# Performance work log

Measured on AMD Instinct MI355X. Metric: run time of the kernel, lower is better.

Reference implementation:

```python
import jax, jax.numpy as jnp
import numpy as np

IN_C, HID, OUT_C, N = 128, 128, 1, 8192


def setup_inputs() -> dict:
    key = jax.random.key(0)
    ks = jax.random.split(key, 16)
    s_in = 1.0 / np.sqrt(IN_C)
    s_h = 1.0 / np.sqrt(HID)
    inp = {
        "x": jax.random.normal(ks[0], (N, IN_C), dtype=jnp.float32),
        "Wq": jax.random.uniform(ks[1], (IN_C, HID), minval=-s_in, maxval=s_in),
        "bq": jnp.zeros((HID,), jnp.float32),
        "Wk": jax.random.uniform(ks[2], (IN_C, HID), minval=-s_in, maxval=s_in),
        "bk": jnp.zeros((HID,), jnp.float32),
        "Wv": jax.random.uniform(ks[3], (IN_C, HID), minval=-s_in, maxval=s_in),
        "bv": jnp.zeros((HID,), jnp.float32),
        "Wskip": jax.random.uniform(ks[4], (IN_C, HID), minval=-s_in, maxval=s_in),
        "bskip": jnp.zeros((HID,), jnp.float32),
        "W1": jax.random.uniform(ks[5], (HID, HID), minval=-s_h, maxval=s_h),
        "b1": jnp.zeros((HID,), jnp.float32),
        "W2": jax.random.uniform(ks[6], (HID, OUT_C), minval=-s_h, maxval=s_h),
        "b2": jnp.zeros((OUT_C,), jnp.float32),
        "k": 7,
    }
    return inp


def _transformer_conv(x, Wq, bq, Wk, bk, Wv, bv, Wskip, bskip):
    # PyG TransformerConv, heads=1, concat=False, root_weight=True, over a
    # complete graph (no self-loops) -> dense attention with masked diagonal.
    q = x @ Wq + bq  # [N, H]
    kk = x @ Wk + bk
    v = x @ Wv + bv
    d = q.shape[-1]
    scores = (q @ kk.T) / jnp.sqrt(jnp.asarray(d, q.dtype))  # [N, N]
    n = x.shape[0]
    eye = jnp.eye(n, dtype=bool)
    scores = jnp.where(eye, -jnp.inf, scores)
    attn = jax.nn.softmax(scores, axis=-1)
    out = attn @ v
    return out + x @ Wskip + bskip


def _knn_indices(h, k):
    # k nearest neighbors (excluding self) in squared-euclidean distance.
    sq = jnp.sum(h * h, axis=1)
    d2 = sq[:, None] + sq[None, :] - 2.0 * (h @ h.T)  # [N, N]
    n = h.shape[0]
    d2 = jnp.where(jnp.eye(n, dtype=bool), jnp.inf, d2)
    _, idx = jax.lax.top_k(-d2, k)  # [N, k] neighbor (source) indices
    return idx


def _gcn_conv(h, idx, W, b, k):
    # Each node has exactly k incoming edges + self-loop => gcn_norm weight
    # is uniformly 1/(k+1) on every edge.
    m = h @ W  # [N, d]
    agg = (m[idx].sum(axis=1) + m) / jnp.asarray(k + 1, h.dtype)
    return agg + b


def reference(x, Wq, bq, Wk, bk, Wv, bv, Wskip, bskip, W1, b1, W2, b2, k):
    h = _transformer_conv(x, Wq, bq, Wk, bk, Wv, bv, Wskip, bskip)  # [N, HID]
    idx = _knn_indices(h, k)  # KNNGraph(k) on embeddings
    h1 = jax.nn.relu(_gcn_conv(h, idx, W1, b1, k))
    out = _gcn_conv(h1, idx, W2, b2, k)  # [N, OUT_C]
    return out
```

## Files before the change

kernel.cpp:

```cpp
#include <hip/hip_runtime.h>
#include <cmath>


typedef unsigned short ushort_t;

constexpr int   NN    = 8192;
constexpr int   DD    = 128;
constexpr int   KNB   = 7;
constexpr int   NL    = 10;
constexpr int   NCAND = 12;
constexpr float SCALE = 0.088388347648318447f;

using bf16x8 = __attribute__((ext_vector_type(8))) short;
using f32x4  = __attribute__((ext_vector_type(4))) float;

#define MFMA16(a, b, c) __builtin_amdgcn_mfma_f32_16x16x32_bf16((a), (b), (c), 0, 0, 0)

__device__ __forceinline__ ushort_t f2b(float f) {
    union { float f; unsigned int u; } v; v.f = f;
    return (ushort_t)((v.u + 0x8000u) >> 16);
}
__device__ __forceinline__ float b2f(ushort_t h) {
    union { unsigned int u; float f; } v; v.u = ((unsigned int)h) << 16;
    return v.f;
}

__device__ __forceinline__ void gload16(const void* g, void* l) {
    __builtin_amdgcn_global_load_lds(
        (const __attribute__((address_space(1))) unsigned int*)g,
        (__attribute__((address_space(3))) unsigned int*)l, 16, 0, 0);
}

__device__ __forceinline__ unsigned umin_(unsigned a, unsigned b) { return a < b ? a : b; }
__device__ __forceinline__ unsigned umax_(unsigned a, unsigned b) { return a > b ? a : b; }

template<int K>
__device__ __forceinline__ void ins_asc(unsigned* a, unsigned x)
{
    #pragma unroll
    for (int p = K - 1; p >= 1; --p)
        a[p] = umin_(umax_(x, a[p - 1]), a[p]);
    a[0] = umin_(a[0], x);
}

__global__ __launch_bounds__(128)
void proj_kernel(const float* __restrict__ x,
                 const float* __restrict__ Wq, const float* __restrict__ bq,
                 const float* __restrict__ Wk, const float* __restrict__ bk,
                 const float* __restrict__ Wv, const float* __restrict__ bv,
                 const float* __restrict__ Ws, const float* __restrict__ bs,
                 ushort_t* __restrict__ Qhi, ushort_t* __restrict__ Qlo,
                 ushort_t* __restrict__ Khi, ushort_t* __restrict__ Klo,
                 float* __restrict__ Vf, float* __restrict__ HS)
{
    __shared__ float xs[4][DD];
    const int i0 = blockIdx.x * 4, t = threadIdx.x;
    #pragma unroll
    for (int r = 0; r < 4; ++r) xs[r][t] = x[(i0 + r) * DD + t];
    __syncthreads();
    float aq[4] = {0,0,0,0}, ak[4] = {0,0,0,0}, av[4] = {0,0,0,0}, ah[4] = {0,0,0,0};
    #pragma unroll 4
    for (int c = 0; c < DD; ++c) {
        const float wq = Wq[c * DD + t], wk = Wk[c * DD + t];
        const float wv = Wv[c * DD + t], ws = Ws[c * DD + t];
        #pragma unroll
        for (int r = 0; r < 4; ++r) {
            const float xv = xs[r][c];
            aq[r] = fmaf(xv, wq, aq[r]); ak[r] = fmaf(xv, wk, ak[r]);
            av[r] = fmaf(xv, wv, av[r]); ah[r] = fmaf(xv, ws, ah[r]);
        }
    }
    #pragma unroll
    for (int r = 0; r < 4; ++r) {
        const int o = (i0 + r) * DD + t;
        const float q = aq[r] + bq[t];
        const float k = ak[r] + bk[t];
        const ushort_t qh = f2b(q); Qhi[o] = qh; Qlo[o] = f2b(q - b2f(qh));
        const ushort_t kh = f2b(k); Khi[o] = kh; Klo[o] = f2b(k - b2f(kh));
        Vf[o] = av[r] + bv[t];
        HS[o] = ah[r] + bs[t];
    }
}

__global__ __launch_bounds__(256)
void vt_kernel(const float* __restrict__ Vf,
               ushort_t* __restrict__ VThi, ushort_t* __restrict__ VTlo)
{
    __shared__ float tile[64 * 132];
    const int k0 = blockIdx.x * 64, t = threadIdx.x;
    #pragma unroll
    for (int p = 0; p < 8; ++p) {
        const int slot = t + p * 256;
        const int r = slot >> 5, c4 = slot & 31;
        *reinterpret_cast<float4*>(&tile[r * 132 + c4 * 4]) =
            *reinterpret_cast<const float4*>(Vf + (k0 + r) * DD + c4 * 4);
    }
    __syncthreads();
    #pragma unroll
    for (int p = 0; p < 4; ++p) {
        const int slot = t + p * 256;
        const int f = slot >> 3, kc = slot & 7;
        ushort_t hh[8], ll[8];
        #pragma unroll
        for (int i = 0; i < 8; ++i) {
            const float v = tile[(kc * 8 + i) * 132 + f];
            hh[i] = f2b(v); ll[i] = f2b(v - b2f(hh[i]));
        }
        *reinterpret_cast<uint4*>(VThi + f * NN + k0 + kc * 8) =
            *reinterpret_cast<const uint4*>(hh);
        *reinterpret_cast<uint4*>(VTlo + f * NN + k0 + kc * 8) =
            *reinterpret_cast<const uint4*>(ll);
    }
}

constexpr int ANS  = 8;
constexpr int AKS  = NN / ANS;
constexpr int BK   = 32;
constexpr int PSTR = 40;
constexpr int KSTR = 136;

__global__ __launch_bounds__(256, 2)
void attn_kernel(const ushort_t* __restrict__ Qhi, const ushort_t* __restrict__ Qlo,
                 const ushort_t* __restrict__ Khg, const ushort_t* __restrict__ Klg,
                 const ushort_t* __restrict__ Vhg, const ushort_t* __restrict__ Vlg,
                 float* __restrict__ Opart, float* __restrict__ lpart)
{
    __shared__ __align__(16) ushort_t Khs[2][BK * DD];
    __shared__ __align__(16) ushort_t Kls[2][BK * DD];
    __shared__ __align__(16) ushort_t Vhs[2][DD * BK];
    __shared__ __align__(16) ushort_t Vls[2][DD * BK];
    __shared__ __align__(16) ushort_t Phs[4][16 * PSTR];
    __shared__ __align__(16) ushort_t Pls[4][16 * PSTR];

    const int t  = threadIdx.x;
    const int w  = t >> 6, l = t & 63;
    const int lc = l & 15, lq = l >> 4;
    const int b  = blockIdx.x;
    const int s  = b >> 6;
    const int qb = b & 63;
    const int i0 = qb * 128;
    const int k0 = s * AKS;
    ushort_t* Pwh = Phs[w];
    ushort_t* Pwl = Pls[w];

    const int lrK = w * 4 + (l >> 4);
    const int kchunk = ((l & 15) ^ (lrK & 7)) * 8;
    const ushort_t* gKh = Khg + (size_t)(k0 + lrK) * DD + kchunk;
    const ushort_t* gKl = Klg + (size_t)(k0 + lrK) * DD + kchunk;
    const int lrV = w * 16 + (l >> 2);
    const int vchunk = ((l & 3) ^ ((l >> 3) & 3)) * 8;
    const ushort_t* gVh = Vhg + (size_t)lrV * NN + k0 + vchunk;
    const ushort_t* gVl = Vlg + (size_t)lrV * NN + k0 + vchunk;

#define STAGE_K(buf, koff) do {                                              \
    gload16(gKh + (size_t)(koff) * DD,        &Khs[buf][(w * 4) * DD]);      \
    gload16(gKh + (size_t)((koff) + 16) * DD, &Khs[buf][(16 + w * 4) * DD]); \
    gload16(gKl + (size_t)(koff) * DD,        &Kls[buf][(w * 4) * DD]);      \
    gload16(gKl + (size_t)((koff) + 16) * DD, &Kls[buf][(16 + w * 4) * DD]); \
  } while (0)
#define STAGE_V(buf, koff) do {                                              \
    gload16(gVh + (koff),                     &Vhs[buf][(w * 16) * BK]);     \
    gload16(gVh + (size_t)64 * NN + (koff),   &Vhs[buf][(64 + w * 16) * BK]);\
    gload16(gVl + (koff),                     &Vls[buf][(w * 16) * BK]);     \
    gload16(gVl + (size_t)64 * NN + (koff),   &Vls[buf][(64 + w * 16) * BK]);\
  } while (0)

    bf16x8 qh[2][4], ql[2][4];
    #pragma unroll
    for (int sub = 0; sub < 2; ++sub) {
        const int row = i0 + w * 32 + sub * 16 + lc;
        #pragma unroll
        for (int kb = 0; kb < 4; ++kb) {
            qh[sub][kb] = *reinterpret_cast<const bf16x8*>(Qhi + row * DD + kb * 32 + lq * 8);
            ql[sub][kb] = *reinterpret_cast<const bf16x8*>(Qlo + row * DD + kb * 32 + lq * 8);
        }
    }

    const f32x4 zz = {0.f, 0.f, 0.f, 0.f};
    f32x4 oacc[2][8];
    #pragma unroll
    for (int sub = 0; sub < 2; ++sub)
        #pragma unroll
        for (int ft = 0; ft < 8; ++ft) oacc[sub][ft] = zz;
    float lrow[2] = {0.f, 0.f};

    bf16x8 pah[2] = {}, pal[2] = {};
    const int vc = (lq ^ ((lc >> 1) & 3)) * 8;

    STAGE_K(0, 0);
    __syncthreads();

    constexpr int NT = AKS / BK;
    for (int it = 0; it < NT; ++it) {
        const int cur = it & 1;
        const int jt  = k0 + it * BK;

        if (it + 1 < NT) STAGE_K(cur ^ 1, (it + 1) * BK);
        STAGE_V(cur, it * BK);

        const ushort_t* Kh = Khs[cur];
        const ushort_t* Kl = Kls[cur];

        f32x4 sacc[2][2];
        #pragma unroll
        for (int sub = 0; sub < 2; ++sub)
            #pragma unroll
            for (int kt = 0; kt < 2; ++kt) sacc[sub][kt] = zz;
        __builtin_amdgcn_s_setprio(1);
        #pragma unroll
        for (int kt = 0; kt < 2; ++kt) {
            const int kro = (kt * 16 + lc) * DD;
            #pragma unroll
            for (int kb = 0; kb < 4; ++kb) {
                const int cp = ((kb * 4 + lq) ^ (lc & 7)) * 8;
                const bf16x8 kh = *reinterpret_cast<const bf16x8*>(&Kh[kro + cp]);
                const bf16x8 kl = *reinterpret_cast<const bf16x8*>(&Kl[kro + cp]);
                #pragma unroll
                for (int sub = 0; sub < 2; ++sub) {
                    sacc[sub][kt] = MFMA16(kh, qh[sub][kb], sacc[sub][kt]);
                    sacc[sub][kt] = MFMA16(kh, ql[sub][kb], sacc[sub][kt]);
                    sacc[sub][kt] = MFMA16(kl, qh[sub][kb], sacc[sub][kt]);
                }
            }
        }
        __builtin_amdgcn_s_setprio(0);

        if (it > 0) {
            const ushort_t* Vh = Vhs[cur ^ 1];
            const ushort_t* Vl = Vls[cur ^ 1];
            __builtin_amdgcn_s_setprio(1);
            #pragma unroll
            for (int ft = 0; ft < 8; ++ft) {
                const bf16x8 vh = *reinterpret_cast<const bf16x8*>(
                    &Vh[(ft * 16 + lc) * BK + vc]);
                const bf16x8 vl = *reinterpret_cast<const bf16x8*>(
                    &Vl[(ft * 16 + lc) * BK + vc]);
                #pragma unroll
                for (int sub = 0; sub < 2; ++sub) {
                    oacc[sub][ft] = MFMA16(pah[sub], vh, oacc[sub][ft]);
                    oacc[sub][ft] = MFMA16(pal[sub], vh, oacc[sub][ft]);
                    oacc[sub][ft] = MFMA16(pah[sub], vl, oacc[sub][ft]);
                }
            }
            __builtin_amdgcn_s_setprio(0);
        }

        if ((jt & ~127) == i0) {
            #pragma unroll
            for (int sub = 0; sub < 2; ++sub) {
                const int gq = i0 + w * 32 + sub * 16 + lc;
                #pragma unroll
                for (int kt = 0; kt < 2; ++kt)
                    #pragma unroll
                    for (int r = 0; r < 4; ++r) {
                        const int gk = jt + kt * 16 + lq * 4 + r;
                        if (gk == gq) sacc[sub][kt][r] = -INFINITY;
                    }
            }
        }
        #pragma unroll
        for (int sub = 0; sub < 2; ++sub) {
            #pragma unroll
            for (int kt = 0; kt < 2; ++kt) {
                unsigned wh[2], wl[2];
                #pragma unroll
                for (int rr = 0; rr < 2; ++rr) {
                    const float p0 = __expf(sacc[sub][kt][rr * 2 + 0] * SCALE);
                    const float p1 = __expf(sacc[sub][kt][rr * 2 + 1] * SCALE);
                    lrow[sub] += p0;
                    lrow[sub] += p1;
                    const ushort_t ph0 = f2b(p0), ph1 = f2b(p1);
                    wh[rr] = (unsigned)ph0 | ((unsigned)ph1 << 16);
                    wl[rr] = (unsigned)f2b(p0 - b2f(ph0)) |
                             ((unsigned)f2b(p1 - b2f(ph1)) << 16);
                }
                const int eo = lc * PSTR + kt * 16 + lq * 4;
                *reinterpret_cast<uint2*>(&Pwh[eo]) = make_uint2(wh[0], wh[1]);
                *reinterpret_cast<uint2*>(&Pwl[eo]) = make_uint2(wl[0], wl[1]);
            }
            pah[sub] = *reinterpret_cast<const bf16x8*>(&Pwh[lc * PSTR + lq * 8]);
            pal[sub] = *reinterpret_cast<const bf16x8*>(&Pwl[lc * PSTR + lq * 8]);
        }

        __syncthreads();
    }
    {
        const ushort_t* Vh = Vhs[(NT - 1) & 1];
        const ushort_t* Vl = Vls[(NT - 1) & 1];
        #pragma unroll
        for (int ft = 0; ft < 8; ++ft) {
            const bf16x8 vh = *reinterpret_cast<const bf16x8*>(
                &Vh[(ft * 16 + lc) * BK + vc]);
            const bf16x8 vl = *reinterpret_cast<const bf16x8*>(
                &Vl[(ft * 16 + lc) * BK + vc]);
            #pragma unroll
            for (int sub = 0; sub < 2; ++sub) {
                oacc[sub][ft] = MFMA16(pah[sub], vh, oacc[sub][ft]);
                oacc[sub][ft] = MFMA16(pal[sub], vh, oacc[sub][ft]);
                oacc[sub][ft] = MFMA16(pah[sub], vl, oacc[sub][ft]);
            }
        }
    }
#undef STAGE_K
#undef STAGE_V

    #pragma unroll
    for (int sub = 0; sub < 2; ++sub) {
        float ps = lrow[sub];
        ps += __shfl_xor(ps, 16, 64);
        ps += __shfl_xor(ps, 32, 64);
        lrow[sub] = ps;
    }
    #pragma unroll
    for (int sub = 0; sub < 2; ++sub) {
        #pragma unroll
        for (int r = 0; r < 4; ++r) {
            const int row = i0 + w * 32 + sub * 16 + lq * 4 + r;
            float* po = Opart + ((size_t)s * NN + row) * DD;
            #pragma unroll
            for (int ft = 0; ft < 8; ++ft) po[ft * 16 + lc] = oacc[sub][ft][r];
        }
        if (l < 16)
            lpart[s * NN + i0 + w * 32 + sub * 16 + l] = lrow[sub];
    }
}

__global__ __launch_bounds__(256)
void attn_merge_kernel(const float* __restrict__ Opart, const float* __restrict__ lpart,
                       const float* __restrict__ HS, float* __restrict__ H,
                       ushort_t* __restrict__ Hhi, float* __restrict__ SQ)
{
    const int t = threadIdx.x;
    const int gid = blockIdx.x * 256 + t;
    const int i = gid >> 5;
    const int f = (gid & 31) * 4;
    float ls = 0.f;
    float4 o = {0.f, 0.f, 0.f, 0.f};
    #pragma unroll
    for (int s = 0; s < ANS; ++s) {
        ls += lpart[s * NN + i];
        const float4 ov = *reinterpret_cast<const float4*>(
            Opart + ((size_t)s * NN + i) * DD + f);
        o.x += ov.x; o.y += ov.y; o.z += ov.z; o.w += ov.w;
    }
    const float4 hs = *reinterpret_cast<const float4*>(HS + i * DD + f);
    const float inv = 1.f / ls;
    float4 h;
    h.x = o.x * inv + hs.x; h.y = o.y * inv + hs.y;
    h.z = o.z * inv + hs.z; h.w = o.w * inv + hs.w;
    *reinterpret_cast<float4*>(H + i * DD + f) = h;
    ushort_t hb[4] = {f2b(h.x), f2b(h.y), f2b(h.z), f2b(h.w)};
    *reinterpret_cast<uint2*>(Hhi + i * DD + f) = *reinterpret_cast<const uint2*>(hb);
    float sq = h.x * h.x + h.y * h.y + h.z * h.z + h.w * h.w;
    sq += __shfl_xor(sq, 1, 64);
    sq += __shfl_xor(sq, 2, 64);
    sq += __shfl_xor(sq, 4, 64);
    sq += __shfl_xor(sq, 8, 64);
    sq += __shfl_xor(sq, 16, 64);
    if ((t & 31) == 0) SQ[i] = sq;
}

constexpr int KNSL = 16;
constexpr int KSL  = NN / KNSL;

__global__ __launch_bounds__(256, 4)
void knn_kernel(const ushort_t* __restrict__ Hhi, const float* __restrict__ SQg,
                unsigned* __restrict__ candV)
{
    __shared__ __align__(16) ushort_t Khi[64 * KSTR];
    __shared__ __align__(16) float sqs[64];

    const int t  = threadIdx.x;
    const int w  = t >> 6, l = t & 63;
    const int lc = l & 15, lq = l >> 4;
    const int b  = blockIdx.x;
    const int s  = b >> 6;
    const int qb = b & 63;
    const int i0 = qb * 128;
    const int k0 = s * KSL;

    const int kr = t >> 4, kc2 = t & 15;

    const int gq0 = i0 + w * 32 + lc;
    const int gq1 = gq0 + 16;
    const float sqi0 = SQg[gq0];
    const float sqi1 = SQg[gq1];

    bf16x8 qf[2][4];
    #pragma unroll
    for (int sub = 0; sub < 2; ++sub) {
        const int row = i0 + w * 32 + sub * 16 + lc;
        #pragma unroll
        for (int kb = 0; kb < 4; ++kb)
            qf[sub][kb] = *reinterpret_cast<const bf16x8*>(Hhi + row * DD + kb * 32 + lq * 8);
    }

    unsigned lists[2][NL];
    #pragma unroll
    for (int sub = 0; sub < 2; ++sub)
        #pragma unroll
        for (int p = 0; p < NL; ++p) lists[sub][p] = 0xFFFFFFFFu;

    uint4 pk[4]; float psq;
    #pragma unroll
    for (int p = 0; p < 4; ++p)
        pk[p] = *reinterpret_cast<const uint4*>(Hhi + (k0 + kr + p * 16) * DD + kc2 * 8);
    psq = (t < 64) ? SQg[k0 + t] : 0.f;

    const f32x4 zz = {0.f, 0.f, 0.f, 0.f};
    for (int jt0 = 0; jt0 < KSL; jt0 += 64) {
        const int jt = k0 + jt0;
        __syncthreads();
        #pragma unroll
        for (int p = 0; p < 4; ++p)
            *reinterpret_cast<uint4*>(&Khi[(kr + p * 16) * KSTR + kc2 * 8]) = pk[p];
        if (t < 64) sqs[t] = psq;
        __syncthreads();
        if (jt0 + 64 < KSL) {
            const int jn = jt + 64;
            #pragma unroll
            for (int p = 0; p < 4; ++p)
                pk[p] = *reinterpret_cast<const uint4*>(Hhi + (jn + kr + p * 16) * DD + kc2 * 8);
            psq = (t < 64) ? SQg[jn + t] : 0.f;
        }

        f32x4 acc[2][4];
        #pragma unroll
        for (int sub = 0; sub < 2; ++sub)
            #pragma unroll
            for (int kt = 0; kt < 4; ++kt) acc[sub][kt] = zz;
        #pragma unroll
        for (int kt = 0; kt < 4; ++kt) {
            #pragma unroll
            for (int kb = 0; kb < 4; ++kb) {
                const bf16x8 kf = *reinterpret_cast<const bf16x8*>(
                    &Khi[(kt * 16 + lc) * KSTR + kb * 32 + lq * 8]);
                acc[0][kt] = MFMA16(kf, qf[0][kb], acc[0][kt]);
                acc[1][kt] = MFMA16(kf, qf[1][kb], acc[1][kt]);
            }
        }

        const bool ovl = ((jt & ~127) == i0);
        #pragma unroll
        for (int kt = 0; kt < 4; ++kt) {
            const float4 sq4 = *reinterpret_cast<const float4*>(&sqs[kt * 16 + lq * 4]);
            const float sqj[4] = {sq4.x, sq4.y, sq4.z, sq4.w};
            #pragma unroll
            for (int r = 0; r < 4; ++r) {
                const int gk = jt + kt * 16 + lq * 4 + r;
                float d0 = fmaf(-2.f, acc[0][kt][r], sqi0 + sqj[r]);
                float d1 = fmaf(-2.f, acc[1][kt][r], sqi1 + sqj[r]);
                if (ovl) {
                    if (gk == gq0) d0 = INFINITY;
                    if (gk == gq1) d1 = INFINITY;
                }
                const unsigned u0 = (__float_as_uint(d0) & 0xFFFFE000u) | (unsigned)gk;
                const unsigned u1 = (__float_as_uint(d1) & 0xFFFFE000u) | (unsigned)gk;
                ins_asc<NL>(lists[0], u0);
                ins_asc<NL>(lists[1], u1);
            }
        }
    }

    __syncthreads();
    unsigned* msw = reinterpret_cast<unsigned*>(Khi) + w * (16 * 4 * NL);
    #pragma unroll
    for (int sub = 0; sub < 2; ++sub) {
        #pragma unroll
        for (int p = 0; p < NL; ++p)
            msw[lc * (4 * NL) + lq * NL + p] = lists[sub][p];
        __syncthreads();
        if (lq == 0) {
            unsigned bk[NL];
            #pragma unroll
            for (int p = 0; p < NL; ++p) bk[p] = msw[lc * (4 * NL) + p];
            #pragma unroll
            for (int o = 1; o < 4; ++o)
                #pragma unroll
                for (int e = 0; e < NL; ++e)
                    ins_asc<NL>(bk, msw[lc * (4 * NL) + o * NL + e]);
            const int node = i0 + w * 32 + sub * 16 + lc;
            #pragma unroll
            for (int p = 0; p < NL; ++p)
                candV[((size_t)s * NL + p) * NN + node] = bk[p];
        }
        __syncthreads();
    }
}

__global__ __launch_bounds__(64)
void knn_merge_kernel(const unsigned* __restrict__ candV, int* __restrict__ CAND)
{
    const int q = blockIdx.x * 64 + threadIdx.x;
    unsigned bk[NCAND];
    #pragma unroll
    for (int p = 0; p < NCAND; ++p) bk[p] = 0xFFFFFFFFu;
    for (int s = 0; s < KNSL; ++s)
        #pragma unroll
        for (int e = 0; e < NL; ++e)
            ins_asc<NCAND>(bk, candV[((size_t)s * NL + e) * NN + q]);
    #pragma unroll
    for (int p = 0; p < NCAND; ++p)
        CAND[q * NCAND + p] = (int)(bk[p] & 8191u);
}

__global__ __launch_bounds__(256)
void rerank_kernel(const float* __restrict__ H, const float* __restrict__ SQ,
                   const int* __restrict__ CAND, int* __restrict__ IDX)
{
    const int t = threadIdx.x;
    const int w = t >> 6, l = t & 63;
    const int node = blockIdx.x * 4 + w;
    const float h0 = H[node * DD + l];
    const float h1 = H[node * DD + 64 + l];
    float dk[NCAND]; int di[NCAND];
    #pragma unroll
    for (int c = 0; c < NCAND; ++c) {
        const int j = CAND[node * NCAND + c];
        float p = h0 * H[j * DD + l] + h1 * H[j * DD + 64 + l];
        p += __shfl_xor(p, 1, 64);
        p += __shfl_xor(p, 2, 64);
        p += __shfl_xor(p, 4, 64);
        p += __shfl_xor(p, 8, 64);
        p += __shfl_xor(p, 16, 64);
        p += __shfl_xor(p, 32, 64);
        dk[c] = SQ[j] - 2.f * p;
        di[c] = j;
    }
    if (l == 0) {
        #pragma unroll
        for (int s = 0; s < KNB; ++s) {
            int best = s;
            #pragma unroll
            for (int c = s + 1; c < NCAND; ++c) {
                const bool lt = (dk[c] < dk[best]) ||
                                (dk[c] == dk[best] && di[c] < di[best]);
                if (lt) best = c;
            }
            const float tk = dk[s]; dk[s] = dk[best]; dk[best] = tk;
            const int   ti = di[s]; di[s] = di[best]; di[best] = ti;
            IDX[node * KNB + s] = di[s];
        }
    }
}

__global__ __launch_bounds__(128)
void mat1_kernel(const float* __restrict__ Hin, const float* __restrict__ W,
                 float* __restrict__ M)
{
    __shared__ float xs[4][DD];
    const int i0 = blockIdx.x * 4, t = threadIdx.x;
    #pragma unroll
    for (int r = 0; r < 4; ++r) xs[r][t] = Hin[(i0 + r) * DD + t];
    __syncthreads();
    float a[4] = {0,0,0,0};
    #pragma unroll 4
    for (int c = 0; c < DD; ++c) {
        const float wv = W[c * DD + t];
        #pragma unroll
        for (int r = 0; r < 4; ++r) a[r] = fmaf(xs[r][c], wv, a[r]);
    }
    #pragma unroll
    for (int r = 0; r < 4; ++r) M[(i0 + r) * DD + t] = a[r];
}

__global__ __launch_bounds__(128)
void g1m2_kernel(const float* __restrict__ M1, const int* __restrict__ IDX,
                 const float* __restrict__ b1, const float* __restrict__ W2,
                 float* __restrict__ M2)
{
    __shared__ float red[128];
    const int i = blockIdx.x, t = threadIdx.x;
    float s = M1[i * DD + t];
    #pragma unroll
    for (int p = 0; p < KNB; ++p) s += M1[IDX[i * KNB + p] * DD + t];
    const float h1 = fmaxf(s * 0.125f + b1[t], 0.f);
    red[t] = h1 * W2[t];
    __syncthreads();
    for (int s2 = 64; s2 > 0; s2 >>= 1) {
        if (t < s2) red[t] += red[t + s2];
        __syncthreads();
    }
    if (t == 0) M2[i] = red[0];
}

__global__ __launch_bounds__(256)
void out_kernel(const float* __restrict__ M2, const int* __restrict__ IDX,
                const float* __restrict__ b2, float* __restrict__ out)
{
    const int i = blockIdx.x * 256 + threadIdx.x;
    if (i < NN) {
        float s = M2[i];
        #pragma unroll
        for (int p = 0; p < KNB; ++p) s += M2[IDX[i * KNB + p]];
        out[i] = s * 0.125f + b2[0];
    }
}

extern "C" void kernel_launch(void* const* d_in, const int* in_sizes, int n_in,
                              void* d_out, int out_size, void* d_ws, size_t ws_size,
                              hipStream_t stream)
{
    const float* x   = (const float*)d_in[0];
    const float* Wq  = (const float*)d_in[1];
    const float* bq  = (const float*)d_in[2];
    const float* Wk  = (const float*)d_in[3];
    const float* bk  = (const float*)d_in[4];
    const float* Wv  = (const float*)d_in[5];
    const float* bv  = (const float*)d_in[6];
    const float* Wsk = (const float*)d_in[7];
    const float* bsk = (const float*)d_in[8];
    const float* W1  = (const float*)d_in[9];
    const float* b1  = (const float*)d_in[10];
    const float* W2  = (const float*)d_in[11];
    const float* b2  = (const float*)d_in[12];

    constexpr size_t MB = 1024 * 1024;
    char* W = (char*)d_ws;
    ushort_t* Qhi  = (ushort_t*)(W + 0 * MB);
    ushort_t* Qlo  = (ushort_t*)(W + 2 * MB);
    ushort_t* Khi  = (ushort_t*)(W + 4 * MB);
    ushort_t* Klo  = (ushort_t*)(W + 6 * MB);
    ushort_t* VThi = (ushort_t*)(W + 8 * MB);
    ushort_t* VTlo = (ushort_t*)(W + 10 * MB);
    float*    HS   = (float*)(W + 12 * MB);
    float*    H    = HS;
    ushort_t* Hhi  = Qhi;
    float* lpart = (float*)(W + 16 * MB);
    float* SQ    = (float*)(W + 16 * MB + 256 * 1024);
    float* M2    = SQ + NN;
    int*   IDX   = (int*)(M2 + NN);
    float*    Vf32  = (float*)(W + 17 * MB);
    float*    Opart = (float*)(W + 17 * MB);
    unsigned* candV = (unsigned*)(W + 17 * MB);
    int*      CAND  = (int*)(W + 23 * MB);
    float*    M1    = (float*)(W + 24 * MB);

    proj_kernel<<<NN / 4, 128, 0, stream>>>(x, Wq, bq, Wk, bk, Wv, bv, Wsk, bsk,
                                            Qhi, Qlo, Khi, Klo, Vf32, HS);
    vt_kernel<<<NN / 64, 256, 0, stream>>>(Vf32, VThi, VTlo);
    attn_kernel<<<ANS * 64, 256, 0, stream>>>(Qhi, Qlo, Khi, Klo, VThi, VTlo,
                                              Opart, lpart);
    attn_merge_kernel<<<(NN * 32) / 256, 256, 0, stream>>>(Opart, lpart, HS, H,
                                                           Hhi, SQ);
    knn_kernel<<<KNSL * 64, 256, 0, stream>>>(Hhi, SQ, candV);
    knn_merge_kernel<<<NN / 64, 64, 0, stream>>>(candV, CAND);
    rerank_kernel<<<NN / 4, 256, 0, stream>>>(H, SQ, CAND, IDX);
    mat1_kernel<<<NN / 4, 128, 0, stream>>>(H, W1, M1);
    g1m2_kernel<<<NN, 128, 0, stream>>>(M1, IDX, b1, W2, M2);
    out_kernel<<<NN / 256, 256, 0, stream>>>(M2, IDX, b2, (float*)d_out);
}
```

Baseline: 335.3 us.

## Deepen K/V prefetch pipeline with explicit waitcnt barriers and packed bf16 conversion

```diff
diff --git a/kernel.cpp b/kernel.cpp
--- a/kernel.cpp
+++ b/kernel.cpp
@@ -164,6 +164,10 @@
     gload16(gVl + (koff),                     &Vls[buf][(w * 16) * BK]);     \
     gload16(gVl + (size_t)64 * NN + (koff),   &Vls[buf][(64 + w * 16) * BK]);\
   } while (0)
+#define LGKM0() asm volatile("s_waitcnt lgkmcnt(0)" ::: "memory")
+#define VMW(n)  asm volatile("s_waitcnt vmcnt(" #n ")" ::: "memory")
+#define BARRIER() do { __builtin_amdgcn_s_barrier(); \
+                       __builtin_amdgcn_sched_barrier(0); } while (0)
 
     bf16x8 qh[2][4], ql[2][4];
     #pragma unroll
@@ -188,18 +192,19 @@
     const int vc = (lq ^ ((lc >> 1) & 3)) * 8;
 
     STAGE_K(0, 0);
-    __syncthreads();
+    STAGE_K(1, BK);
+    STAGE_V(0, 0);
+    VMW(8);
+    BARRIER();
 
     constexpr int NT = AKS / BK;
     for (int it = 0; it < NT; ++it) {
+        const int jt  = k0 + it * BK;
         const int cur = it & 1;
-        const int jt  = k0 + it * BK;
-
-        if (it + 1 < NT) STAGE_K(cur ^ 1, (it + 1) * BK);
-        STAGE_V(cur, it * BK);
-
         const ushort_t* Kh = Khs[cur];
         const ushort_t* Kl = Kls[cur];
+        const ushort_t* Vph = Vhs[cur ^ 1];
+        const ushort_t* Vpl = Vls[cur ^ 1];
 
         f32x4 sacc[2][2];
         #pragma unroll
@@ -226,15 +231,13 @@
         __builtin_amdgcn_s_setprio(0);
 
         if (it > 0) {
-            const ushort_t* Vh = Vhs[cur ^ 1];
-            const ushort_t* Vl = Vls[cur ^ 1];
             __builtin_amdgcn_s_setprio(1);
             #pragma unroll
             for (int ft = 0; ft < 8; ++ft) {
                 const bf16x8 vh = *reinterpret_cast<const bf16x8*>(
-                    &Vh[(ft * 16 + lc) * BK + vc]);
+                    &Vph[(ft * 16 + lc) * BK + vc]);
                 const bf16x8 vl = *reinterpret_cast<const bf16x8*>(
-                    &Vl[(ft * 16 + lc) * BK + vc]);
+                    &Vpl[(ft * 16 + lc) * BK + vc]);
                 #pragma unroll
                 for (int sub = 0; sub < 2; ++sub) {
                     oacc[sub][ft] = MFMA16(pah[sub], vh, oacc[sub][ft]);
@@ -244,6 +247,12 @@
             }
             __builtin_amdgcn_s_setprio(0);
         }
+
+        LGKM0();
+        BARRIER();
+
+        if (it <= NT - 3) STAGE_K(cur, (it + 2) * BK);
+        if (it <= NT - 2) STAGE_V(cur ^ 1, (it + 1) * BK);
 
         if ((jt & ~127) == i0) {
             #pragma unroll
@@ -269,10 +278,16 @@
                     const float p1 = __expf(sacc[sub][kt][rr * 2 + 1] * SCALE);
                     lrow[sub] += p0;
                     lrow[sub] += p1;
-                    const ushort_t ph0 = f2b(p0), ph1 = f2b(p1);
-                    wh[rr] = (unsigned)ph0 | ((unsigned)ph1 << 16);
-                    wl[rr] = (unsigned)f2b(p0 - b2f(ph0)) |
-                             ((unsigned)f2b(p1 - b2f(ph1)) << 16);
+                    unsigned hpk;
+                    asm("v_cvt_pk_bf16_f32 %0, %1, %2"
+                        : "=v"(hpk) : "v"(p0), "v"(p1));
+                    wh[rr] = hpk;
+                    const float h0 = __uint_as_float(hpk << 16);
+                    const float h1 = __uint_as_float(hpk & 0xFFFF0000u);
+                    unsigned lpk;
+                    asm("v_cvt_pk_bf16_f32 %0, %1, %2"
+                        : "=v"(lpk) : "v"(p0 - h0), "v"(p1 - h1));
+                    wl[rr] = lpk;
                 }
                 const int eo = lc * PSTR + kt * 16 + lq * 4;
                 *reinterpret_cast<uint2*>(&Pwh[eo]) = make_uint2(wh[0], wh[1]);
@@ -282,7 +297,10 @@
             pal[sub] = *reinterpret_cast<const bf16x8*>(&Pwl[lc * PSTR + lq * 8]);
         }
 
-        __syncthreads();
+        if (it <= NT - 3)      { VMW(8); }
+        else if (it == NT - 2) { VMW(4); }
+        else                   { VMW(0); }
+        BARRIER();
     }
     {
         const ushort_t* Vh = Vhs[(NT - 1) & 1];
@@ -303,6 +321,9 @@
     }
 #undef STAGE_K
 #undef STAGE_V
+#undef LGKM0
+#undef VMW
+#undef BARRIER
 
     #pragma unroll
     for (int sub = 0; sub < 2; ++sub) {
```

Result: no change. 333.4 us (-0.6%).
